# Optimization experiments

Measured on AMD Instinct MI355X. Metric: run time of the kernel, lower is better.

The kernel has to match this reference:

```python
import jax, jax.numpy as jnp
import numpy as np

EPS = 1e-5
NEG_SLOPE = 0.2  # DGL GATConv default leaky_relu slope


def conv1d_same(x, w, b):
    # x: [N, Cin, T], w: [Cout, Cin, K]
    y = jax.lax.conv_general_dilated(x, w, (1,), 'SAME',
                                     dimension_numbers=('NCW', 'OIW', 'NCW'))
    return y + b[None, :, None]


def gated_conv(x, w1, b1, w2, b2, w3, b3):
    # Temporal_Gated_Conv: relu(conv1(x)*sigmoid(conv2(x)) + conv3(x))
    return jax.nn.relu(conv1d_same(x, w1, b1) * jax.nn.sigmoid(conv1d_same(x, w2, b2))
                       + conv1d_same(x, w3, b3))


def bn3(x, g, b):
    # BatchNorm1d on [N, C, T]: stats over (N, T), training mode (batch stats)
    m = jnp.mean(x, (0, 2), keepdims=True)
    v = jnp.var(x, (0, 2), keepdims=True)
    return (x - m) * jax.lax.rsqrt(v + EPS) * g[None, :, None] + b[None, :, None]


def bn2(x, g, b):
    # BatchNorm1d on [N, F]: stats over N
    m = jnp.mean(x, 0, keepdims=True)
    v = jnp.var(x, 0, keepdims=True)
    return (x - m) * jax.lax.rsqrt(v + EPS) * g[None, :] + b[None, :]


def setup_inputs() -> dict:
    key = jax.random.key(0)
    ks = jax.random.split(key, 24)
    N, C, T, H, DEG = 20000, 32, 8, 4, 16
    F = C * T          # GAT in/out feats per head = 256
    E = N * DEG
    s = 0.05
    inp = {
        'X': jax.random.normal(ks[0], (N, C, T), jnp.float32),
        'src': jax.random.randint(ks[1], (E,), 0, N, jnp.int32),
        'dst': jax.random.randint(ks[2], (E,), 0, N, jnp.int32),
        # residual_proj: Conv1d(C->C, k=1)
        'rp_w': jax.random.normal(ks[3], (C, C, 1), jnp.float32) * s,
        'rp_b': jnp.zeros((C,), jnp.float32),
        # gated_conv1: three Conv1d(C->C, k=3)
        'g1_w1': jax.random.normal(ks[4], (C, C, 3), jnp.float32) * s,
        'g1_b1': jnp.zeros((C,), jnp.float32),
        'g1_w2': jax.random.normal(ks[5], (C, C, 3), jnp.float32) * s,
        'g1_b2': jnp.zeros((C,), jnp.float32),
        'g1_w3': jax.random.normal(ks[6], (C, C, 3), jnp.float32) * s,
        'g1_b3': jnp.zeros((C,), jnp.float32),
        'bn0_g': jnp.ones((C,), jnp.float32),
        'bn0_b': jnp.zeros((C,), jnp.float32),
        # GATConv: fc [H*F, F], attn_l/attn_r [H, F], bias [H*F]
        'gat_w': jax.random.normal(ks[7], (H * F, F), jnp.float32) * s,
        'attn_l': jax.random.normal(ks[8], (H, F), jnp.float32) * s,
        'attn_r': jax.random.normal(ks[9], (H, F), jnp.float32) * s,
        'gat_bias': jnp.zeros((H * F,), jnp.float32),
        'bn1_g': jnp.ones((H * F,), jnp.float32),
        'bn1_b': jnp.zeros((H * F,), jnp.float32),
        # gated_conv2: three Conv1d(C*H -> C, k=3)
        'g2_w1': jax.random.normal(ks[10], (C, C * H, 3), jnp.float32) * s,
        'g2_b1': jnp.zeros((C,), jnp.float32),
        'g2_w2': jax.random.normal(ks[11], (C, C * H, 3), jnp.float32) * s,
        'g2_b2': jnp.zeros((C,), jnp.float32),
        'g2_w3': jax.random.normal(ks[12], (C, C * H, 3), jnp.float32) * s,
        'g2_b3': jnp.zeros((C,), jnp.float32),
        'bn2_g': jnp.ones((C,), jnp.float32),
        'bn2_b': jnp.zeros((C,), jnp.float32),
    }
    return inp


def reference(X, src, dst, rp_w, rp_b, g1_w1, g1_b1, g1_w2, g1_b2, g1_w3, g1_b3,
              bn0_g, bn0_b, gat_w, attn_l, attn_r, gat_bias, bn1_g, bn1_b,
              g2_w1, g2_b1, g2_w2, g2_b2, g2_w3, g2_b3, bn2_g, bn2_b):
    N, C, T = X.shape
    H, F = attn_l.shape

    residual = conv1d_same(X, rp_w, rp_b)                      # [N, C, T]
    x = gated_conv(X, g1_w1, g1_b1, g1_w2, g1_b2, g1_w3, g1_b3)
    x = bn3(x, bn0_g, bn0_b)
    x = x.reshape(N, C * T)                                    # row-major flatten == torch .view

    # --- DGL GATConv (feat_drop=attn_drop=0, concat heads, ReLU activation) ---
    h = (x @ gat_w.T).reshape(N, H, F)                         # fc projection
    el = jnp.sum(h * attn_l, -1)                               # [N, H]
    er = jnp.sum(h * attn_r, -1)                               # [N, H]
    e = jax.nn.leaky_relu(el[src] + er[dst], NEG_SLOPE)        # [E, H]
    # segment softmax over incoming edges of each dst node
    m = jax.ops.segment_max(e, dst, num_segments=N)            # [N, H]
    ee = jnp.exp(e - m[dst])
    den = jax.ops.segment_sum(ee, dst, num_segments=N)         # [N, H]
    alpha = ee / den[dst]                                      # [E, H]
    rst = jax.ops.segment_sum(alpha[:, :, None] * h[src], dst, num_segments=N)  # [N, H, F]
    rst = jax.nn.relu(rst + gat_bias.reshape(H, F))

    x = rst.reshape(N, H * F)                                  # concat heads
    x = bn2(x, bn1_g, bn1_b)
    x = x.reshape(N, (H * F) // T, T)                          # [N, C*H, T]
    x = gated_conv(x, g2_w1, g2_b1, g2_w2, g2_b2, g2_w3, g2_b3)
    x = bn3(x, bn2_g, bn2_b)
    x = jax.nn.relu(x + residual)                              # self.last=True, dropout=0
    return x
```

## Files before the change

### kernel.cpp

```cpp
#include <hip/hip_runtime.h>
#include <stdint.h>

#define NN 20000
#define NE 320000

typedef unsigned short us16;
typedef __attribute__((ext_vector_type(8))) short short8;
typedef __attribute__((ext_vector_type(4))) float f32x4;

union U4 { uint4 v; us16 s[8]; unsigned u[4]; };
union U2 { uint2 v; us16 s[4]; };

__device__ __forceinline__ float b2f(us16 u){ return __uint_as_float(((unsigned)u)<<16); }
__device__ __forceinline__ us16 f2b(float f){
  unsigned u = __float_as_uint(f);
  u += 0x7fffu + ((u>>16)&1u);
  return (us16)(u>>16);
}

__global__ __launch_bounds__(256) void k_misc(
    const float* __restrict__ gatw, us16* __restrict__ Wb,
    const float* __restrict__ w1, const float* __restrict__ w2, const float* __restrict__ w3,
    us16* __restrict__ Wt,
    const float* __restrict__ c1w1, const float* __restrict__ c1w2, const float* __restrict__ c1w3,
    const float* __restrict__ rp_w, us16* __restrict__ Wt1,
    const float* __restrict__ attnl, const float* __restrict__ attnr,
    float* __restrict__ wl, float* __restrict__ wr,
    const int* __restrict__ dst, int* __restrict__ counts)
{
  const int b = blockIdx.x, tid = threadIdx.x;
  if(b < 256){
    int i = b*256 + tid;
    float4 v = *(const float4*)(gatw + (size_t)i*4);
    U2 o;
    o.s[0]=f2b(v.x); o.s[1]=f2b(v.y); o.s[2]=f2b(v.z); o.s[3]=f2b(v.w);
    *(uint2*)(Wb + (size_t)i*4) = o.v;
  } else if(b < 400){
    int i = (b-256)*256 + tid;
    int s = i/12288, rem = i%12288;
    int co3 = rem>>7, ci = rem&127;
    const float* w = (co3<32) ? w1 : (co3<64) ? w2 : w3;
    Wt[i] = f2b(w[(co3&31)*384 + ci*3 + s]);
  } else if(b < 448){
    int i = (b-400)*256 + tid;
    int s = i>>12, rem = i&4095;
    int co3 = rem>>5, ci = rem&31;
    float v;
    if(co3 < 96){
      const float* w = (co3<32) ? c1w1 : (co3<64) ? c1w2 : c1w3;
      v = w[(co3&31)*96 + ci*3 + s];
    } else {
      v = (s==1) ? rp_w[(co3-96)*32 + ci] : 0.f;
    }
    Wt1[i] = f2b(v);
  } else if(b < 480){
    int bb = b-448;
    int sel = bb>>4, hd = (bb>>2)&3, fq = bb&3;
    const float* attn = sel ? attnr : attnl;
    int k = tid;
    float s = 0.f;
    int f0 = fq*64;
    #pragma unroll 8
    for(int f=f0; f<f0+64; f++)
      s = fmaf(attn[hd*256+f], gatw[(size_t)(hd*256+f)*256 + k], s);
    atomicAdd(&((sel ? wr : wl)[hd*256+k]), s);
  } else {
    int e = (b-480)*256 + tid;
    if(e < NE) atomicAdd(&counts[dst[e]], 1);
  }
}

__global__ __launch_bounds__(256) void k_gemm1(
    const float* __restrict__ X, const us16* __restrict__ Wt1,
    const float* __restrict__ b1, const float* __restrict__ b2, const float* __restrict__ b3,
    const float* __restrict__ rp_b,
    us16* __restrict__ gc1, us16* __restrict__ resid,
    float* __restrict__ bn0_sum, float* __restrict__ bn0_sq,
    const int* __restrict__ counts, int* __restrict__ offsets, int* __restrict__ cursor)
{
  __shared__ float smemF[16896];
  __shared__ float redS[32], redQ[32];
  const int tid = threadIdx.x;
  if(blockIdx.x < 1250){
    us16* As = (us16*)smemF;
    us16* Bs = As + 6400;
    float* Cs = smemF;
    if(tid<32){ redS[tid]=0.f; redQ[tid]=0.f; }
    const int node0 = blockIdx.x*16;
    const int lane = tid&63, wv = tid>>6;
    const int wm = wv&1, wn = wv>>1;
    const int mrow = lane&15, kg = (lane>>4)*8;
    for(int idx=tid; idx<1024; idx+=256){
      int n = idx>>6, rem = idx&63, slot = (rem>>5)*9, ci = rem&31;
      As[n*400 + slot*40 + ci] = 0;
    }
    #pragma unroll
    for(int i=0;i<4;i++){
      int idx = i*256 + tid;
      int n = idx>>6, rem = idx&63, ci = rem>>1, tq = rem&1;
      float4 xv = *(const float4*)(X + (size_t)(node0+n)*256 + ci*8 + tq*4);
      us16* p = &As[n*400 + (tq*4+1)*40 + ci];
      p[0]   = f2b(xv.x);
      p[40]  = f2b(xv.y);
      p[80]  = f2b(xv.z);
      p[120] = f2b(xv.w);
    }
    #pragma unroll
    for(int i=0;i<6;i++){
      int c = i*256 + tid;
      int s = c>>9, rem = c&511, co = rem>>2, cq = rem&3;
      *(uint4*)&Bs[s*5120 + co*40 + cq*8] = *(const uint4*)(Wt1 + s*4096 + co*32 + cq*8);
    }
    __syncthreads();
    f32x4 acc[4][4] = {};
    #pragma unroll
    for(int s=0; s<3; s++){
      short8 af[4], bfr[4];
      #pragma unroll
      for(int i=0;i<4;i++){
        int r = wm*64 + i*16 + mrow;
        af[i] = *(const short8*)&As[(r>>3)*400 + ((r&7)+s)*40 + kg];
      }
      #pragma unroll
      for(int j=0;j<4;j++)
        bfr[j] = *(const short8*)&Bs[s*5120 + (wn*64 + j*16 + mrow)*40 + kg];
      #pragma unroll
      for(int i=0;i<4;i++){
        #pragma unroll
        for(int j=0;j<4;j++)
          acc[i][j] = __builtin_amdgcn_mfma_f32_16x16x32_bf16(af[i], bfr[j], acc[i][j], 0, 0, 0);
      }
    }
    __syncthreads();
    #pragma unroll
    for(int i=0;i<4;i++){
      #pragma unroll
      for(int j=0;j<4;j++){
        #pragma unroll
        for(int r=0;r<4;r++)
          Cs[(wm*64 + i*16 + (lane>>4)*4 + r)*132 + wn*64 + j*16 + (lane&15)] = acc[i][j][r];
      }
    }
    __syncthreads();
    const int co = tid&31, rg = tid>>5;
    const float bb1=b1[co], bb2=b2[co], bb3=b3[co], bbr=rp_b[co];
    float s=0.f, q=0.f;
    #pragma unroll
    for(int half=0; half<2; half++){
      U4 ov, rv;
      #pragma unroll
      for(int t=0;t<8;t++){
        int r = rg*16 + half*8 + t;
        float c1 = Cs[r*132 + co]      + bb1;
        float c2 = Cs[r*132 + co + 32] + bb2;
        float c3 = Cs[r*132 + co + 64] + bb3;
        float rr = Cs[r*132 + co + 96] + bbr;
        float sg = 1.f/(1.f+__expf(-c2));
        float v = fmaf(c1, sg, c3);
        v = v>0.f ? v : 0.f;
        s += v; q += v*v;
        ov.s[t] = f2b(v);
        rv.s[t] = f2b(rr);
      }
      int node = node0 + rg*2 + half;
      *(uint4*)(gc1   + (size_t)node*256 + co*8) = ov.v;
      *(uint4*)(resid + (size_t)node*256 + co*8) = rv.v;
    }
    atomicAdd(&redS[co], s); atomicAdd(&redQ[co], q);
    __syncthreads();
    if(tid<32)      atomicAdd(&bn0_sum[tid], redS[tid]);
    else if(tid<64) atomicAdd(&bn0_sq[tid-32], redQ[tid-32]);
  } else {
    us16* cnt  = (us16*)smemF;
    int*  wsum = (int*)(smemF + 12800);
    for(int r=0;r<79;r++){
      int idx = r*256 + tid;
      cnt[idx] = (idx<NN) ? (us16)counts[idx] : (us16)0;
    }
    __syncthreads();
    const int base = tid*79;
    int s = 0;
    for(int j=0;j<79;j++) s += cnt[base+j];
    wsum[tid] = s;
    __syncthreads();
    for(int off=1; off<256; off<<=1){
      int t = (tid>=off) ? wsum[tid-off] : 0;
      __syncthreads();
      wsum[tid] += t;
      __syncthreads();
    }
    int excl = wsum[tid] - s;
    for(int j=0;j<79;j++){
      int idx = base+j;
      if(idx<NN){
        offsets[idx]=excl; cursor[idx]=excl;
        excl += cnt[idx];
      }
    }
    if(tid==255) offsets[NN] = wsum[255];
  }
}

__global__ __launch_bounds__(256) void k_eler2(const us16* __restrict__ gc1,
    const float* __restrict__ bn0_sum, const float* __restrict__ bn0_sq,
    const float* __restrict__ bn0g, const float* __restrict__ bn0b,
    const float* __restrict__ wl, const float* __restrict__ wr,
    float* __restrict__ el, float* __restrict__ er)
{
  __shared__ float sa[32], sb[32];
  const int tid = threadIdx.x;
  if(tid<32){
    float m = bn0_sum[tid]*(1.f/160000.f);
    float v = bn0_sq[tid]*(1.f/160000.f) - m*m;
    float a = bn0g[tid]*rsqrtf(v + 1e-5f);
    sa[tid] = a; sb[tid] = bn0b[tid] - m*a;
  }
  __syncthreads();
  const int wv = tid>>6, lane = tid&63;
  const int node = blockIdx.x*4 + wv;
  U2 g; g.v = *(const uint2*)(gc1 + (size_t)node*256 + lane*4);
  const float a = sa[lane>>1], b = sb[lane>>1];
  float xv[4];
  #pragma unroll
  for(int j=0;j<4;j++) xv[j] = fmaf(a, b2f(g.s[j]), b);
  float res[8];
  #pragma unroll
  for(int hd=0; hd<4; hd++){
    float4 lv = *(const float4*)(wl + hd*256 + lane*4);
    float4 rv = *(const float4*)(wr + hd*256 + lane*4);
    res[hd]   = xv[0]*lv.x + xv[1]*lv.y + xv[2]*lv.z + xv[3]*lv.w;
    res[4+hd] = xv[0]*rv.x + xv[1]*rv.y + xv[2]*rv.z + xv[3]*rv.w;
  }
  #pragma unroll
  for(int o=32;o;o>>=1){
    #pragma unroll
    for(int k=0;k<8;k++) res[k] += __shfl_xor(res[k], o, 64);
  }
  if(lane==0){
    #pragma unroll
    for(int hd=0;hd<4;hd++){ el[node*4+hd]=res[hd]; er[node*4+hd]=res[4+hd]; }
  }
}

__global__ __launch_bounds__(256) void k_scatter(const int* __restrict__ src, const int* __restrict__ dst,
    int* __restrict__ cursor, int* __restrict__ esrc,
    const float* __restrict__ el, const float* __restrict__ er,
    float* __restrict__ ew)
{
  int e = blockIdx.x*256 + threadIdx.x;
  if(e < NE){
    int s = src[e], d = dst[e];
    int pos = atomicAdd(&cursor[d], 1);
    esrc[pos] = s;
    float4 lv = *(const float4*)(el + s*4);
    float4 rv = *(const float4*)(er + d*4);
    float4 sc;
    sc.x = lv.x+rv.x; sc.x = sc.x>0.f ? sc.x : 0.2f*sc.x;
    sc.y = lv.y+rv.y; sc.y = sc.y>0.f ? sc.y : 0.2f*sc.y;
    sc.z = lv.z+rv.z; sc.z = sc.z>0.f ? sc.z : 0.2f*sc.z;
    sc.w = lv.w+rv.w; sc.w = sc.w>0.f ? sc.w : 0.2f*sc.w;
    *(float4*)(ew + (size_t)pos*4) = sc;
  }
}

__global__ __launch_bounds__(256) void k_agg2(
    const int* __restrict__ offsets, const int* __restrict__ esrc,
    const float* __restrict__ ew, const us16* __restrict__ gc1,
    const float* __restrict__ bn0_sum, const float* __restrict__ bn0_sq,
    const float* __restrict__ bn0g, const float* __restrict__ bn0b,
    us16* __restrict__ Axg)
{
  const int tid = threadIdx.x;
  const int wv = tid>>6, lane = tid&63;
  const int node = blockIdx.x*4 + wv;
  const int ch = lane>>1;
  float mmn = bn0_sum[ch]*(1.f/160000.f);
  float vvn = bn0_sq[ch]*(1.f/160000.f) - mmn*mmn;
  float sa = bn0g[ch]*rsqrtf(vvn + 1e-5f);
  float sb = bn0b[ch] - mmn*sa;
  const int beg = offsets[node];
  const int deg = offsets[node+1] - beg;
  const int h = lane>>4, i0 = lane&15;
  float m = -3.0e38f;
  for(int i=i0; i<deg; i+=16) m = fmaxf(m, ew[(size_t)(beg+i)*4 + h]);
  m = fmaxf(m, __shfl_xor(m,1,64)); m = fmaxf(m, __shfl_xor(m,2,64));
  m = fmaxf(m, __shfl_xor(m,4,64)); m = fmaxf(m, __shfl_xor(m,8,64));
  float den = 0.f;
  for(int i=i0; i<deg; i+=16) den += __expf(ew[(size_t)(beg+i)*4 + h] - m);
  den += __shfl_xor(den,1,64); den += __shfl_xor(den,2,64);
  den += __shfl_xor(den,4,64); den += __shfl_xor(den,8,64);
  const float m0=__shfl(m,0,64),   m1=__shfl(m,16,64),  m2=__shfl(m,32,64),  m3=__shfl(m,48,64);
  const float d0=__shfl(den,0,64), d1=__shfl(den,16,64),d2=__shfl(den,32,64),d3=__shfl(den,48,64);
  const float v0=d0>0.f?1.f/d0:0.f, v1=d1>0.f?1.f/d1:0.f,
              v2=d2>0.f?1.f/d2:0.f, v3=d3>0.f?1.f/d3:0.f;
  float a0c[4]={},a1c[4]={},a2c[4]={},a3c[4]={};
  #pragma unroll 4
  for(int j=0; j<deg; j++){
    int pos = beg+j;
    float4 w4 = *(const float4*)(ew + (size_t)pos*4);
    int sN = esrc[pos];
    U2 hv; hv.v = *(const uint2*)(gc1 + (size_t)sN*256 + lane*4);
    float e0 = __expf(w4.x-m0)*v0;
    float e1 = __expf(w4.y-m1)*v1;
    float e2 = __expf(w4.z-m2)*v2;
    float e3 = __expf(w4.w-m3)*v3;
    #pragma unroll
    for(int kk=0;kk<4;kk++){
      float x = b2f(hv.s[kk]);
      a0c[kk] = fmaf(e0,x,a0c[kk]);
      a1c[kk] = fmaf(e1,x,a1c[kk]);
      a2c[kk] = fmaf(e2,x,a2c[kk]);
      a3c[kk] = fmaf(e3,x,a3c[kk]);
    }
  }
  const float sbi = sb * ((deg>0)?1.f:0.f);
  U2 o0,o1,o2,o3;
  #pragma unroll
  for(int kk=0;kk<4;kk++){
    o0.s[kk]=f2b(fmaf(sa,a0c[kk],sbi));
    o1.s[kk]=f2b(fmaf(sa,a1c[kk],sbi));
    o2.s[kk]=f2b(fmaf(sa,a2c[kk],sbi));
    o3.s[kk]=f2b(fmaf(sa,a3c[kk],sbi));
  }
  *(uint2*)(Axg + ((size_t)node)*256            + lane*4) = o0.v;
  *(uint2*)(Axg + ((size_t)NN + node)*256       + lane*4) = o1.v;
  *(uint2*)(Axg + ((size_t)2*NN + node)*256     + lane*4) = o2.v;
  *(uint2*)(Axg + ((size_t)3*NN + node)*256     + lane*4) = o3.v;
}

__global__ __launch_bounds__(256) void k_gemm3(const us16* __restrict__ Axg, const us16* __restrict__ Wb,
    const float* __restrict__ gbias, us16* __restrict__ rst,
    float* __restrict__ bn1_sum, float* __restrict__ bn1_sq)
{
  __shared__ us16 As[128*40];
  __shared__ us16 Bs[128*40];
  const int tid = threadIdx.x;
  const int row0 = blockIdx.x*128;
  const int cb   = blockIdx.y*128;
  const int hd   = blockIdx.z;
  const us16* A = Axg + (size_t)hd*NN*256;
  const us16* B = Wb  + (size_t)(hd*256 + cb)*256;
  const int lane = tid&63, wv = tid>>6;
  const int wm = wv&1, wn = wv>>1;
  const int mrow = lane&15, kg = (lane>>4)*8;
  f32x4 acc[4][4] = {};
  for(int k0=0; k0<256; k0+=32){
    #pragma unroll
    for(int i=0;i<2;i++){
      int chunk = i*256 + tid;
      int row = chunk>>2, cc = chunk&3;
      int g = row0 + row;
      uint4 av; av.x=0;av.y=0;av.z=0;av.w=0;
      if(g < NN) av = *(const uint4*)(A + (size_t)g*256 + k0 + cc*8);
      *(uint4*)&As[row*40 + cc*8] = av;
      *(uint4*)&Bs[row*40 + cc*8] = *(const uint4*)(B + (size_t)row*256 + k0 + cc*8);
    }
    __syncthreads();
    short8 af[4], bfr[4];
    #pragma unroll
    for(int i=0;i<4;i++) af[i]  = *(const short8*)&As[(wm*64 + i*16 + mrow)*40 + kg];
    #pragma unroll
    for(int j=0;j<4;j++) bfr[j] = *(const short8*)&Bs[(wn*64 + j*16 + mrow)*40 + kg];
    #pragma unroll
    for(int i=0;i<4;i++){
      #pragma unroll
      for(int j=0;j<4;j++)
        acc[i][j] = __builtin_amdgcn_mfma_f32_16x16x32_bf16(af[i], bfr[j], acc[i][j], 0, 0, 0);
    }
    __syncthreads();
  }
  float gb[4];
  #pragma unroll
  for(int j=0;j<4;j++)
    gb[j] = gbias[hd*256 + cb + wn*64 + j*16 + (lane&15)];
  float cs[4]={}, cq[4]={};
  #pragma unroll
  for(int i=0;i<4;i++){
    #pragma unroll
    for(int j=0;j<4;j++){
      #pragma unroll
      for(int r=0;r<4;r++){
        int g = row0 + wm*64 + i*16 + (lane>>4)*4 + r;
        if(g < NN){
          float v = acc[i][j][r] + gb[j];
          v = v>0.f ? v : 0.f;
          rst[(size_t)g*1024 + hd*256 + cb + wn*64 + j*16 + (lane&15)] = f2b(v);
          cs[j] += v; cq[j] += v*v;
        }
      }
    }
  }
  #pragma unroll
  for(int j=0;j<4;j++){
    cs[j] += __shfl_xor(cs[j],16,64); cs[j] += __shfl_xor(cs[j],32,64);
    cq[j] += __shfl_xor(cq[j],16,64); cq[j] += __shfl_xor(cq[j],32,64);
  }
  if(lane < 16){
    #pragma unroll
    for(int j=0;j<4;j++){
      int col = hd*256 + cb + wn*64 + j*16 + lane;
      atomicAdd(&bn1_sum[col], cs[j]);
      atomicAdd(&bn1_sq[col],  cq[j]);
    }
  }
}

__global__ __launch_bounds__(256) void k_gemm2(
    const us16* __restrict__ rst, const us16* __restrict__ Wt,
    const float* __restrict__ bn1_sum, const float* __restrict__ bn1_sq,
    const float* __restrict__ bn1g, const float* __restrict__ bn1b,
    const float* __restrict__ b1, const float* __restrict__ b2, const float* __restrict__ b3,
    us16* __restrict__ y2, float* __restrict__ bn2_sum, float* __restrict__ bn2_sq)
{
  __shared__ float smemF[12800];
  float* s1a = smemF;
  float* s1b = smemF + 1024;
  us16* As = (us16*)(smemF + 2048);
  us16* Bs = As + 11520;
  float* Cs = smemF;
  __shared__ float redS[32], redQ[32];
  const int tid = threadIdx.x;
  if(tid<32){ redS[tid]=0.f; redQ[tid]=0.f; }
  const int node0 = blockIdx.x*16;
  const int lane = tid&63, wv = tid>>6;
  const int wm = wv&1, wn = wv>>1;
  const int mrow = lane&15, kg = (lane>>4)*8;
  for(int f=tid; f<1024; f+=256){
    float m = bn1_sum[f]*(1.f/20000.f);
    float v = bn1_sq[f]*(1.f/20000.f) - m*m;
    float a = bn1g[f]*rsqrtf(v + 1e-5f);
    int l = (f&7)*128 + (f>>3);
    s1a[l] = a; s1b[l] = bn1b[f] - m*a;
  }
  for(int idx=tid; idx<2048; idx+=256){
    int n = idx>>7, rem = idx&127, slot = (rem>>6)*9, ci = rem&63;
    As[n*720 + slot*72 + ci] = 0;
  }
  __syncthreads();
  f32x4 acc[4][3] = {};
  for(int kc=0; kc<2; kc++){
    if(kc) __syncthreads();
    #pragma unroll
    for(int i=0;i<4;i++){
      int idx = i*256 + tid;
      int n = idx>>6, cil = idx&63;
      int ci = kc*64 + cil;
      U4 in; in.v = *(const uint4*)(rst + (size_t)(node0+n)*1024 + ci*8);
      us16* p = &As[n*720 + 72 + cil];
      #pragma unroll
      for(int t=0;t<8;t++){
        float a = s1a[t*128+ci], b = s1b[t*128+ci];
        p[t*72] = f2b(fmaf(a, b2f(in.s[t]), b));
      }
    }
    for(int s=0; s<3; s++){
      if(s) __syncthreads();
      #pragma unroll
      for(int i=0;i<3;i++){
        int chunk = i*256 + tid;
        int brow = chunk>>3, cc = chunk&7;
        *(uint4*)&Bs[brow*72 + cc*8] =
          *(const uint4*)(Wt + s*12288 + brow*128 + kc*64 + cc*8);
      }
      __syncthreads();
      #pragma unroll
      for(int kk=0; kk<64; kk+=32){
        short8 af[4], bfr[3];
        #pragma unroll
        for(int i=0;i<4;i++){
          int r = wm*64 + i*16 + mrow;
          af[i] = *(const short8*)&As[(r>>3)*720 + ((r&7)+s)*72 + kk + kg];
        }
        #pragma unroll
        for(int j=0;j<3;j++)
          bfr[j] = *(const short8*)&Bs[(wn*48 + j*16 + mrow)*72 + kk + kg];
        #pragma unroll
        for(int i=0;i<4;i++){
          #pragma unroll
          for(int j=0;j<3;j++)
            acc[i][j] = __builtin_amdgcn_mfma_f32_16x16x32_bf16(af[i], bfr[j], acc[i][j], 0, 0, 0);
        }
      }
    }
  }
  __syncthreads();
  #pragma unroll
  for(int i=0;i<4;i++){
    #pragma unroll
    for(int j=0;j<3;j++){
      #pragma unroll
      for(int r=0;r<4;r++)
        Cs[(wm*64 + i*16 + (lane>>4)*4 + r)*100 + wn*48 + j*16 + (lane&15)] = acc[i][j][r];
    }
  }
  __syncthreads();
  const int co = tid&31, rg = tid>>5;
  const float bb1=b1[co], bb2=b2[co], bb3=b3[co];
  float s=0.f, q=0.f;
  #pragma unroll
  for(int half=0; half<2; half++){
    U4 ov;
    #pragma unroll
    for(int t=0;t<8;t++){
      int r = rg*16 + half*8 + t;
      float c1 = Cs[r*100 + co]      + bb1;
      float c2 = Cs[r*100 + co + 32] + bb2;
      float c3 = Cs[r*100 + co + 64] + bb3;
      float sg = 1.f/(1.f+__expf(-c2));
      float v = fmaf(c1, sg, c3);
      v = v>0.f ? v : 0.f;
      s += v; q += v*v;
      ov.s[t] = f2b(v);
    }
    int node = node0 + rg*2 + half;
    *(uint4*)(y2 + (size_t)node*256 + co*8) = ov.v;
  }
  atomicAdd(&redS[co], s); atomicAdd(&redQ[co], q);
  __syncthreads();
  if(tid<32)      atomicAdd(&bn2_sum[tid], redS[tid]);
  else if(tid<64) atomicAdd(&bn2_sq[tid-32], redQ[tid-32]);
}

__global__ __launch_bounds__(256) void k_final(const us16* __restrict__ y2,
    const float* __restrict__ bn2_sum, const float* __restrict__ bn2_sq,
    const float* __restrict__ bn2g, const float* __restrict__ bn2b,
    const us16* __restrict__ resid, float* __restrict__ out)
{
  __shared__ float fa[32], fb[32];
  const int tid = threadIdx.x;
  if(tid<32){
    float m = bn2_sum[tid]*(1.f/160000.f);
    float v = bn2_sq[tid]*(1.f/160000.f) - m*m;
    float a = bn2g[tid]*rsqrtf(v + 1e-5f);
    fa[tid] = a; fb[tid] = bn2b[tid] - m*a;
  }
  __syncthreads();
  size_t base = ((size_t)blockIdx.x*256 + tid)*8;
  int ch = (int)((base>>3)&31);
  float a = fa[ch], b = fb[ch];
  U4 yv, rv;
  yv.v = *(const uint4*)(y2+base);
  rv.v = *(const uint4*)(resid+base);
  float4 o0, o1;
  float vv[8];
  #pragma unroll
  for(int j=0;j<8;j++){
    float v = fmaf(a, b2f(yv.s[j]), b) + b2f(rv.s[j]);
    vv[j] = v>0.f ? v : 0.f;
  }
  o0.x=vv[0]; o0.y=vv[1]; o0.z=vv[2]; o0.w=vv[3];
  o1.x=vv[4]; o1.y=vv[5]; o1.z=vv[6]; o1.w=vv[7];
  *(float4*)(out+base)   = o0;
  *(float4*)(out+base+4) = o1;
}

extern "C" void kernel_launch(void* const* d_in, const int* in_sizes, int n_in,
                              void* d_out, int out_size, void* d_ws, size_t ws_size,
                              hipStream_t stream)
{
  const float* X    = (const float*)d_in[0];
  const int*  src   = (const int*)d_in[1];
  const int*  dst   = (const int*)d_in[2];
  const float* rp_w = (const float*)d_in[3];
  const float* rp_b = (const float*)d_in[4];
  const float* g1w1 = (const float*)d_in[5];
  const float* g1b1 = (const float*)d_in[6];
  const float* g1w2 = (const float*)d_in[7];
  const float* g1b2 = (const float*)d_in[8];
  const float* g1w3 = (const float*)d_in[9];
  const float* g1b3 = (const float*)d_in[10];
  const float* bn0g = (const float*)d_in[11];
  const float* bn0b = (const float*)d_in[12];
  const float* gatw = (const float*)d_in[13];
  const float* attnl= (const float*)d_in[14];
  const float* attnr= (const float*)d_in[15];
  const float* gbias= (const float*)d_in[16];
  const float* bn1g = (const float*)d_in[17];
  const float* bn1b = (const float*)d_in[18];
  const float* g2w1 = (const float*)d_in[19];
  const float* g2b1 = (const float*)d_in[20];
  const float* g2w2 = (const float*)d_in[21];
  const float* g2b2 = (const float*)d_in[22];
  const float* g2w3 = (const float*)d_in[23];
  const float* g2b3 = (const float*)d_in[24];
  const float* bn2g = (const float*)d_in[25];
  const float* bn2b = (const float*)d_in[26];
  float* out = (float*)d_out;
  (void)in_sizes; (void)n_in; (void)out_size; (void)ws_size;

  char* w = (char*)d_ws;
  float* bn0_sum = (float*)w;
  float* bn0_sq  = bn0_sum + 32;
  float* bn1_sum = bn0_sum + 64;
  float* bn1_sq  = bn1_sum + 1024;
  float* bn2_sum = bn1_sq  + 1024;
  float* bn2_sq  = bn2_sum + 32;
  float* wl      = bn2_sq + 32;
  float* wr      = wl + 1024;
  int*   counts  = (int*)(wr + 1024);
  size_t zeroBytes = (size_t)((char*)(counts + NN) - w);
  int*   offsets = counts + NN;
  int*   cursor  = offsets + 20004;
  int*   esrc    = cursor + NN;
  float* el      = (float*)(esrc + NE);
  float* er      = el + NN*4;
  float* ew      = er + NN*4;
  us16*  wb      = (us16*)(ew + (size_t)NE*4);
  us16*  resid   = wb + 262144;
  us16*  gc1     = resid + 5120000;
  us16*  Axg     = gc1   + 5120000;
  us16*  rst     = Axg   + 20480000;
  us16*  Wt      = rst   + 20480000;
  us16*  Wt1     = Wt    + 36864;
  us16*  y2      = gc1;

  hipMemsetAsync(d_ws, 0, zeroBytes, stream);
  k_misc<<<1730, 256, 0, stream>>>(gatw, wb, g2w1, g2w2, g2w3, Wt,
                                   g1w1, g1w2, g1w3, rp_w, Wt1,
                                   attnl, attnr, wl, wr, dst, counts);
  k_gemm1<<<1251, 256, 0, stream>>>(X, Wt1, g1b1, g1b2, g1b3, rp_b,
                                    gc1, resid, bn0_sum, bn0_sq,
                                    counts, offsets, cursor);
  k_eler2<<<5000, 256, 0, stream>>>(gc1, bn0_sum, bn0_sq, bn0g, bn0b, wl, wr, el, er);
  k_scatter<<<1250, 256, 0, stream>>>(src, dst, cursor, esrc, el, er, ew);
  k_agg2<<<5000, 256, 0, stream>>>(offsets, esrc, ew, gc1, bn0_sum, bn0_sq, bn0g, bn0b, Axg);
  k_gemm3<<<dim3(157, 2, 4), 256, 0, stream>>>(Axg, wb, gbias, rst, bn1_sum, bn1_sq);
  k_gemm2<<<1250, 256, 0, stream>>>(rst, Wt, bn1_sum, bn1_sq, bn1g, bn1b,
                                    g2b1, g2b2, g2b3, y2, bn2_sum, bn2_sq);
  k_final<<<2500, 256, 0, stream>>>(y2, bn2_sum, bn2_sq, bn2g, bn2b, resid, out);
}
```

Before: 380.4 us.

## Shrink gemm1 LDS, epilogue from registers, and use wave-shuffle scan for offsets

```diff
diff --git a/kernel.cpp b/kernel.cpp
--- a/kernel.cpp
+++ b/kernel.cpp
@@ -78,17 +78,16 @@
     float* __restrict__ bn0_sum, float* __restrict__ bn0_sq,
     const int* __restrict__ counts, int* __restrict__ offsets, int* __restrict__ cursor)
 {
-  __shared__ float smemF[16896];
+  __shared__ float smemF[5760];
   __shared__ float redS[32], redQ[32];
+  __shared__ int wred[4];
   const int tid = threadIdx.x;
   if(blockIdx.x < 1250){
     us16* As = (us16*)smemF;
     us16* Bs = As + 6400;
-    float* Cs = smemF;
     if(tid<32){ redS[tid]=0.f; redQ[tid]=0.f; }
     const int node0 = blockIdx.x*16;
     const int lane = tid&63, wv = tid>>6;
-    const int wm = wv&1, wn = wv>>1;
     const int mrow = lane&15, kg = (lane>>4)*8;
     for(int idx=tid; idx<1024; idx+=256){
       int n = idx>>6, rem = idx&63, slot = (rem>>5)*9, ci = rem&31;
@@ -105,99 +104,135 @@
       p[80]  = f2b(xv.z);
       p[120] = f2b(xv.w);
     }
-    #pragma unroll
-    for(int i=0;i<6;i++){
-      int c = i*256 + tid;
-      int s = c>>9, rem = c&511, co = rem>>2, cq = rem&3;
-      *(uint4*)&Bs[s*5120 + co*40 + cq*8] = *(const uint4*)(Wt1 + s*4096 + co*32 + cq*8);
+    f32x4 acc[2][8] = {};
+    for(int s=0; s<3; s++){
+      if(s) __syncthreads();
+      #pragma unroll
+      for(int i=0;i<2;i++){
+        int c = i*256 + tid;
+        int co = c>>2, cq = c&3;
+        *(uint4*)&Bs[co*40 + cq*8] = *(const uint4*)(Wt1 + s*4096 + co*32 + cq*8);
+      }
+      __syncthreads();
+      short8 af[2], bfr[8];
+      #pragma unroll
+      for(int i=0;i<2;i++){
+        int r = wv*32 + i*16 + mrow;
+        af[i] = *(const short8*)&As[(r>>3)*400 + ((r&7)+s)*40 + kg];
+      }
+      #pragma unroll
+      for(int j=0;j<8;j++)
+        bfr[j] = *(const short8*)&Bs[(j*16 + mrow)*40 + kg];
+      #pragma unroll
+      for(int i=0;i<2;i++){
+        #pragma unroll
+        for(int j=0;j<8;j++)
+          acc[i][j] = __builtin_amdgcn_mfma_f32_16x16x32_bf16(af[i], bfr[j], acc[i][j], 0, 0, 0);
+      }
     }
     __syncthreads();
-    f32x4 acc[4][4] = {};
-    #pragma unroll
-    for(int s=0; s<3; s++){
-      short8 af[4], bfr[4];
-      #pragma unroll
-      for(int i=0;i<4;i++){
-        int r = wm*64 + i*16 + mrow;
-        af[i] = *(const short8*)&As[(r>>3)*400 + ((r&7)+s)*40 + kg];
-      }
-      #pragma unroll
-      for(int j=0;j<4;j++)
-        bfr[j] = *(const short8*)&Bs[s*5120 + (wn*64 + j*16 + mrow)*40 + kg];
-      #pragma unroll
-      for(int i=0;i<4;i++){
-        #pragma unroll
-        for(int j=0;j<4;j++)
-          acc[i][j] = __builtin_amdgcn_mfma_f32_16x16x32_bf16(af[i], bfr[j], acc[i][j], 0, 0, 0);
-      }
+    us16* Og = (us16*)smemF;
+    us16* Or = Og + 4096;
+    const int coA = lane&15, coB = coA+16;
+    const float b1A=b1[coA], b2A=b2[coA], b3A=b3[coA], brA=rp_b[coA];
+    const float b1B=b1[coB], b2B=b2[coB], b3B=b3[coB], brB=rp_b[coB];
+    float sA=0.f, qA=0.f, sB=0.f, qB=0.f;
+    const int g = lane>>4;
+    #pragma unroll
+    for(int i=0;i<2;i++){
+      int node = wv*4 + i*2 + (g>>1);
+      int t0 = (g&1)*4;
+      U2 pA, pB, rA2, rB2;
+      #pragma unroll
+      for(int r=0;r<4;r++){
+        float c1 = acc[i][0][r]+b1A, c2 = acc[i][2][r]+b2A, c3 = acc[i][4][r]+b3A;
+        float rr = acc[i][6][r]+brA;
+        float sg = 1.f/(1.f+__expf(-c2));
+        float v = fmaf(c1,sg,c3); v = v>0.f ? v : 0.f;
+        sA += v; qA += v*v;
+        pA.s[r]=f2b(v); rA2.s[r]=f2b(rr);
+        c1 = acc[i][1][r]+b1B; c2 = acc[i][3][r]+b2B; c3 = acc[i][5][r]+b3B;
+        rr = acc[i][7][r]+brB;
+        sg = 1.f/(1.f+__expf(-c2));
+        v = fmaf(c1,sg,c3); v = v>0.f ? v : 0.f;
+        sB += v; qB += v*v;
+        pB.s[r]=f2b(v); rB2.s[r]=f2b(rr);
+      }
+      *(uint2*)&Og[node*256 + coA*8 + t0] = pA.v;
+      *(uint2*)&Og[node*256 + coB*8 + t0] = pB.v;
+      *(uint2*)&Or[node*256 + coA*8 + t0] = rA2.v;
+      *(uint2*)&Or[node*256 + coB*8 + t0] = rB2.v;
+    }
+    sA += __shfl_xor(sA,16,64); sA += __shfl_xor(sA,32,64);
+    qA += __shfl_xor(qA,16,64); qA += __shfl_xor(qA,32,64);
+    sB += __shfl_xor(sB,16,64); sB += __shfl_xor(sB,32,64);
+    qB += __shfl_xor(qB,16,64); qB += __shfl_xor(qB,32,64);
+    if(lane < 16){
+      atomicAdd(&redS[coA], sA); atomicAdd(&redQ[coA], qA);
+      atomicAdd(&redS[coB], sB); atomicAdd(&redQ[coB], qB);
     }
     __syncthreads();
     #pragma unroll
-    for(int i=0;i<4;i++){
-      #pragma unroll
-      for(int j=0;j<4;j++){
-        #pragma unroll
-        for(int r=0;r<4;r++)
-          Cs[(wm*64 + i*16 + (lane>>4)*4 + r)*132 + wn*64 + j*16 + (lane&15)] = acc[i][j][r];
-      }
-    }
-    __syncthreads();
-    const int co = tid&31, rg = tid>>5;
-    const float bb1=b1[co], bb2=b2[co], bb3=b3[co], bbr=rp_b[co];
-    float s=0.f, q=0.f;
-    #pragma unroll
-    for(int half=0; half<2; half++){
-      U4 ov, rv;
-      #pragma unroll
-      for(int t=0;t<8;t++){
-        int r = rg*16 + half*8 + t;
-        float c1 = Cs[r*132 + co]      + bb1;
-        float c2 = Cs[r*132 + co + 32] + bb2;
-        float c3 = Cs[r*132 + co + 64] + bb3;
-        float rr = Cs[r*132 + co + 96] + bbr;
-        float sg = 1.f/(1.f+__expf(-c2));
-        float v = fmaf(c1, sg, c3);
-        v = v>0.f ? v : 0.f;
-        s += v; q += v*v;
-        ov.s[t] = f2b(v);
-        rv.s[t] = f2b(rr);
-      }
-      int node = node0 + rg*2 + half;
-      *(uint4*)(gc1   + (size_t)node*256 + co*8) = ov.v;
-      *(uint4*)(resid + (size_t)node*256 + co*8) = rv.v;
-    }
-    atomicAdd(&redS[co], s); atomicAdd(&redQ[co], q);
-    __syncthreads();
+    for(int i=0;i<2;i++){
+      int idx = i*256 + tid;
+      *(uint4*)(gc1   + (size_t)node0*256 + (size_t)idx*8) = *(const uint4*)&Og[idx*8];
+      *(uint4*)(resid + (size_t)node0*256 + (size_t)idx*8) = *(const uint4*)&Or[idx*8];
+    }
     if(tid<32)      atomicAdd(&bn0_sum[tid], redS[tid]);
     else if(tid<64) atomicAdd(&bn0_sq[tid-32], redQ[tid-32]);
   } else {
-    us16* cnt  = (us16*)smemF;
-    int*  wsum = (int*)(smemF + 12800);
-    for(int r=0;r<79;r++){
-      int idx = r*256 + tid;
-      cnt[idx] = (idx<NN) ? (us16)counts[idx] : (us16)0;
-    }
-    __syncthreads();
-    const int base = tid*79;
-    int s = 0;
-    for(int j=0;j<79;j++) s += cnt[base+j];
-    wsum[tid] = s;
-    __syncthreads();
-    for(int off=1; off<256; off<<=1){
-      int t = (tid>=off) ? wsum[tid-off] : 0;
+    const int lane = tid&63, wv = tid>>6;
+    int running = 0;
+    int4 cur;
+    {
+      int idx = tid*4;
+      cur = *(const int4*)(counts + idx);
+    }
+    for(int t=0; t<20; t++){
+      int4 nxt; nxt.x=0; nxt.y=0; nxt.z=0; nxt.w=0;
+      if(t < 19){
+        int idx = (t+1)*1024 + tid*4;
+        if(idx+3 < NN) nxt = *(const int4*)(counts + idx);
+        else {
+          if(idx   < NN) nxt.x = counts[idx];
+          if(idx+1 < NN) nxt.y = counts[idx+1];
+          if(idx+2 < NN) nxt.z = counts[idx+2];
+          if(idx+3 < NN) nxt.w = counts[idx+3];
+        }
+      }
+      int s = cur.x + cur.y + cur.z + cur.w;
+      int incl = s;
+      #pragma unroll
+      for(int off=1; off<64; off<<=1){
+        int v = __shfl_up(incl, off, 64);
+        if(lane >= off) incl += v;
+      }
+      if(lane==63) wred[wv] = incl;
       __syncthreads();
-      wsum[tid] += t;
+      int woff = 0, btot = 0;
+      #pragma unroll
+      for(int w2=0; w2<4; w2++){
+        int x = wred[w2];
+        btot += x;
+        if(w2 < wv) woff += x;
+      }
+      int e0 = running + woff + incl - s;
+      int idx = t*1024 + tid*4;
+      int4 o; o.x=e0; o.y=e0+cur.x; o.z=o.y+cur.y; o.w=o.z+cur.z;
+      if(idx+3 < NN){
+        *(int4*)(offsets+idx) = o;
+        *(int4*)(cursor+idx)  = o;
+      } else {
+        if(idx   < NN){ offsets[idx]  =o.x; cursor[idx]  =o.x; }
+        if(idx+1 < NN){ offsets[idx+1]=o.y; cursor[idx+1]=o.y; }
+        if(idx+2 < NN){ offsets[idx+2]=o.z; cursor[idx+2]=o.z; }
+        if(idx+3 < NN){ offsets[idx+3]=o.w; cursor[idx+3]=o.w; }
+      }
+      running += btot;
+      cur = nxt;
       __syncthreads();
     }
-    int excl = wsum[tid] - s;
-    for(int j=0;j<79;j++){
-      int idx = base+j;
-      if(idx<NN){
-        offsets[idx]=excl; cursor[idx]=excl;
-        excl += cnt[idx];
-      }
-    }
-    if(tid==255) offsets[NN] = wsum[255];
+    if(tid==0) offsets[NN] = running;
   }
 }
 
```

Result: faster. 363.4 us (-4.5%).
